# Kernel tuning notes

Hardware: AMD Instinct MI355X
Metric: run time of the kernel (lower is better)

## Reference

```python
import jax, jax.numpy as jnp
import numpy as np


def setup_inputs() -> dict:
    key = jax.random.key(0)
    k1, k2 = jax.random.split(key)
    A, B, N, M, K = 8, 16, 1024, 1024, 64
    u = jax.random.normal(k1, (A, B, N, K), dtype=jnp.float32)
    v = jax.random.normal(k2, (A, B, M, K), dtype=jnp.float32)
    return {"u": u, "v": v}


def reference(u, v):
    # to_norm = u @ v^T has shape (A,B,N,M); we only need its row/col sums.
    # sum over M of (u @ v^T) = u @ sum_m(v);  sum over N = v @ sum_n(u).
    v_sum = v.sum(axis=2)                     # (A,B,K)
    u_sum = u.sum(axis=2)                     # (A,B,K)
    row_sum = jnp.einsum('abnk,abk->abn', u, v_sum)   # to_norm.sum(dim=3)
    col_sum = jnp.einsum('abmk,abk->abm', v, u_sum)   # to_norm.sum(dim=2)
    left_mul = jax.nn.relu(jnp.sign(row_sum))[..., None]   # (A,B,N,1)
    right_mul = jax.nn.relu(jnp.sign(col_sum))[..., None]  # (A,B,M,1)
    return (left_mul * u, right_mul * v)
```

## Files before the change

### kernel.cpp

```cpp
#include <hip/hip_runtime.h>


#define NBATCH 128
#define NROW   1024
#define KDIM   64
#define ELEMS_PER_TENSOR (128ull * 1024ull * 64ull)

typedef float floatx4 __attribute__((ext_vector_type(4)));

__global__ __launch_bounds__(1024)
void fused_local_kernel(const float* __restrict__ u,
                        const float* __restrict__ v,
                        float* __restrict__ out) {
    const int bid   = blockIdx.x;
    const int batch = bid >> 1;
    const int half  = bid & 1;
    const int tid   = threadIdx.x;
    const int k4    = tid & 15;
    const int rg    = tid >> 4;
    const int wave  = tid >> 6;

    const float4* ub = (const float4*)(u + (size_t)batch * NROW * KDIM);
    const float4* vb = (const float4*)(v + (size_t)batch * NROW * KDIM);

    const int r_own0 = half * 512 + rg;
    const int r_oth0 = (1 - half) * 512 + rg;

    float4 ur[8], vr[8];
    float4 su = make_float4(0.f, 0.f, 0.f, 0.f);
    float4 sv = make_float4(0.f, 0.f, 0.f, 0.f);
    #pragma unroll
    for (int i = 0; i < 8; ++i) {
        size_t io = (size_t)(r_own0 + 64 * i) * 16 + k4;
        ur[i] = ub[io];
        vr[i] = vb[io];
        su.x += ur[i].x; su.y += ur[i].y; su.z += ur[i].z; su.w += ur[i].w;
        sv.x += vr[i].x; sv.y += vr[i].y; sv.z += vr[i].z; sv.w += vr[i].w;
    }
    #pragma unroll
    for (int i = 0; i < 8; ++i) {
        size_t ix = (size_t)(r_oth0 + 64 * i) * 16 + k4;
        float4 a = ub[ix];
        float4 b = vb[ix];
        su.x += a.x; su.y += a.y; su.z += a.z; su.w += a.w;
        sv.x += b.x; sv.y += b.y; sv.z += b.z; sv.w += b.w;
    }

    su.x += __shfl_xor(su.x, 16); su.y += __shfl_xor(su.y, 16);
    su.z += __shfl_xor(su.z, 16); su.w += __shfl_xor(su.w, 16);
    su.x += __shfl_xor(su.x, 32); su.y += __shfl_xor(su.y, 32);
    su.z += __shfl_xor(su.z, 32); su.w += __shfl_xor(su.w, 32);
    sv.x += __shfl_xor(sv.x, 16); sv.y += __shfl_xor(sv.y, 16);
    sv.z += __shfl_xor(sv.z, 16); sv.w += __shfl_xor(sv.w, 16);
    sv.x += __shfl_xor(sv.x, 32); sv.y += __shfl_xor(sv.y, 32);
    sv.z += __shfl_xor(sv.z, 32); sv.w += __shfl_xor(sv.w, 32);

    __shared__ float4 red_u[16][16];
    __shared__ float4 red_v[16][16];
    __shared__ float4 fsum[2][16];
    if ((tid & 63) < 16) {
        red_u[wave][k4] = su;
        red_v[wave][k4] = sv;
    }
    __syncthreads();

    if (tid < 32) {
        const int which = tid >> 4;
        const int c     = tid & 15;
        float4 t = make_float4(0.f, 0.f, 0.f, 0.f);
        if (which == 0) {
            #pragma unroll
            for (int i = 0; i < 16; ++i) {
                float4 b = red_v[i][c];
                t.x += b.x; t.y += b.y; t.z += b.z; t.w += b.w;
            }
        } else {
            #pragma unroll
            for (int i = 0; i < 16; ++i) {
                float4 a = red_u[i][c];
                t.x += a.x; t.y += a.y; t.z += a.z; t.w += a.w;
            }
        }
        fsum[which][c] = t;
    }
    __syncthreads();

    const float4 vs = fsum[0][k4];
    const float4 us = fsum[1][k4];

    float* ou = out + (size_t)batch * NROW * KDIM;
    float* ov = out + ELEMS_PER_TENSOR + (size_t)batch * NROW * KDIM;

    #pragma unroll
    for (int i = 0; i < 8; ++i) {
        size_t io = (size_t)(r_own0 + 64 * i) * 16 + k4;

        float pu = ur[i].x * vs.x + ur[i].y * vs.y + ur[i].z * vs.z + ur[i].w * vs.w;
        pu += __shfl_xor(pu, 1);
        pu += __shfl_xor(pu, 2);
        pu += __shfl_xor(pu, 4);
        pu += __shfl_xor(pu, 8);
        float mu = (pu > 0.f) ? 1.f : 0.f;
        floatx4 outu = { ur[i].x * mu, ur[i].y * mu, ur[i].z * mu, ur[i].w * mu };
        __builtin_nontemporal_store(outu, (floatx4*)(ou + io * 4));

        float pv = vr[i].x * us.x + vr[i].y * us.y + vr[i].z * us.z + vr[i].w * us.w;
        pv += __shfl_xor(pv, 1);
        pv += __shfl_xor(pv, 2);
        pv += __shfl_xor(pv, 4);
        pv += __shfl_xor(pv, 8);
        float mv = (pv > 0.f) ? 1.f : 0.f;
        floatx4 outv = { vr[i].x * mv, vr[i].y * mv, vr[i].z * mv, vr[i].w * mv };
        __builtin_nontemporal_store(outv, (floatx4*)(ov + io * 4));
    }
}

extern "C" void kernel_launch(void* const* d_in, const int* in_sizes, int n_in,
                              void* d_out, int out_size, void* d_ws, size_t ws_size,
                              hipStream_t stream) {
    const float* u = (const float*)d_in[0];
    const float* v = (const float*)d_in[1];
    float* out = (float*)d_out;

    fused_local_kernel<<<dim3(256), dim3(1024), 0, stream>>>(u, v, out);
}
```

Before: 118.4 us.

## Split fused kernel into column-sum and mask kernels with XCD-aware block mapping

Replaces the single fused kernel, where each block redundantly summed the other half of its batch, with a column-sum kernel that writes partial sums to workspace and a mask kernel that combines them and applies the sign mask. Block IDs are remapped so that the blocks of one batch land on the same XCD, to improve cache locality when the inputs are reread. This removes the duplicated half reads but adds a second launch and a full reread of u and v. The old fused kernel is kept as a fallback when no workspace is available.

```diff
diff --git a/kernel.cpp b/kernel.cpp
--- a/kernel.cpp
+++ b/kernel.cpp
@@ -6,42 +6,40 @@
 #define KDIM   64
 #define ELEMS_PER_TENSOR (128ull * 1024ull * 64ull)
 
+#define WS_PAYLOAD_FLOATS (NBATCH * 2 * 2 * 64)
+#define WS_BYTES ((size_t)WS_PAYLOAD_FLOATS * 4)
+
 typedef float floatx4 __attribute__((ext_vector_type(4)));
 
+__device__ __forceinline__ void decode_bid(int bid, int& batch, int& half) {
+    const int xcd  = bid & 7;
+    const int slot = bid >> 3;
+    batch = xcd * 16 + (slot >> 1);
+    half  = slot & 1;
+}
+
 __global__ __launch_bounds__(1024)
-void fused_local_kernel(const float* __restrict__ u,
-                        const float* __restrict__ v,
-                        float* __restrict__ out) {
-    const int bid   = blockIdx.x;
-    const int batch = bid >> 1;
-    const int half  = bid & 1;
-    const int tid   = threadIdx.x;
-    const int k4    = tid & 15;
-    const int rg    = tid >> 4;
-    const int wave  = tid >> 6;
+void colsum_kernel(const float* __restrict__ u,
+                   const float* __restrict__ v,
+                   float4* __restrict__ ws) {
+    int batch, half;
+    decode_bid(blockIdx.x, batch, half);
+    const int tid  = threadIdx.x;
+    const int k4   = tid & 15;
+    const int rg   = tid >> 4;
+    const int wave = tid >> 6;
 
     const float4* ub = (const float4*)(u + (size_t)batch * NROW * KDIM);
     const float4* vb = (const float4*)(v + (size_t)batch * NROW * KDIM);
-
-    const int r_own0 = half * 512 + rg;
-    const int r_oth0 = (1 - half) * 512 + rg;
-
-    float4 ur[8], vr[8];
+    const int r0 = half * 512 + rg;
+
     float4 su = make_float4(0.f, 0.f, 0.f, 0.f);
     float4 sv = make_float4(0.f, 0.f, 0.f, 0.f);
     #pragma unroll
     for (int i = 0; i < 8; ++i) {
-        size_t io = (size_t)(r_own0 + 64 * i) * 16 + k4;
-        ur[i] = ub[io];
-        vr[i] = vb[io];
-        su.x += ur[i].x; su.y += ur[i].y; su.z += ur[i].z; su.w += ur[i].w;
-        sv.x += vr[i].x; sv.y += vr[i].y; sv.z += vr[i].z; sv.w += vr[i].w;
-    }
-    #pragma unroll
-    for (int i = 0; i < 8; ++i) {
-        size_t ix = (size_t)(r_oth0 + 64 * i) * 16 + k4;
-        float4 a = ub[ix];
-        float4 b = vb[ix];
+        size_t io = (size_t)(r0 + 64 * i) * 16 + k4;
+        float4 a = ub[io];
+        float4 b = vb[io];
         su.x += a.x; su.y += a.y; su.z += a.z; su.w += a.w;
         sv.x += b.x; sv.y += b.y; sv.z += b.z; sv.w += b.w;
     }
@@ -57,7 +55,6 @@
 
     __shared__ float4 red_u[16][16];
     __shared__ float4 red_v[16][16];
-    __shared__ float4 fsum[2][16];
     if ((tid & 63) < 16) {
         red_u[wave][k4] = su;
         red_v[wave][k4] = sv;
@@ -81,20 +78,44 @@
                 t.x += a.x; t.y += a.y; t.z += a.z; t.w += a.w;
             }
         }
-        fsum[which][c] = t;
-    }
-    __syncthreads();
-
-    const float4 vs = fsum[0][k4];
-    const float4 us = fsum[1][k4];
-
-    float* ou = out + (size_t)batch * NROW * KDIM;
-    float* ov = out + ELEMS_PER_TENSOR + (size_t)batch * NROW * KDIM;
-
-    #pragma unroll
-    for (int i = 0; i < 8; ++i) {
-        size_t io = (size_t)(r_own0 + 64 * i) * 16 + k4;
-
+        ws[(((size_t)batch * 2 + half) * 2 + which) * 16 + c] = t;
+    }
+}
+
+__global__ __launch_bounds__(1024)
+void mask_kernel(const float* __restrict__ u,
+                 const float* __restrict__ v,
+                 float* __restrict__ out,
+                 const float4* __restrict__ ws) {
+    int batch, half;
+    decode_bid(blockIdx.x, batch, half);
+    const int tid = threadIdx.x;
+    const int k4  = tid & 15;
+    const int rg  = tid >> 4;
+
+    const float4 vs0 = ws[(((size_t)batch * 2 + 0) * 2 + 0) * 16 + k4];
+    const float4 vs1 = ws[(((size_t)batch * 2 + 1) * 2 + 0) * 16 + k4];
+    const float4 us0 = ws[(((size_t)batch * 2 + 0) * 2 + 1) * 16 + k4];
+    const float4 us1 = ws[(((size_t)batch * 2 + 1) * 2 + 1) * 16 + k4];
+    const float4 vs = make_float4(vs0.x + vs1.x, vs0.y + vs1.y,
+                                  vs0.z + vs1.z, vs0.w + vs1.w);
+    const float4 us = make_float4(us0.x + us1.x, us0.y + us1.y,
+                                  us0.z + us1.z, us0.w + us1.w);
+
+    const size_t boff = (size_t)batch * NROW * KDIM;
+    const float4* ub = (const float4*)(u + boff);
+    const float4* vb = (const float4*)(v + boff);
+    float* ou = out + boff;
+    float* ov = out + ELEMS_PER_TENSOR + boff;
+    const int r0 = half * 512 + rg;
+
+    float4 ur[8];
+    #pragma unroll
+    for (int i = 0; i < 8; ++i)
+        ur[i] = ub[(size_t)(r0 + 64 * i) * 16 + k4];
+    #pragma unroll
+    for (int i = 0; i < 8; ++i) {
+        size_t io = (size_t)(r0 + 64 * i) * 16 + k4;
         float pu = ur[i].x * vs.x + ur[i].y * vs.y + ur[i].z * vs.z + ur[i].w * vs.w;
         pu += __shfl_xor(pu, 1);
         pu += __shfl_xor(pu, 2);
@@ -103,7 +124,15 @@
         float mu = (pu > 0.f) ? 1.f : 0.f;
         floatx4 outu = { ur[i].x * mu, ur[i].y * mu, ur[i].z * mu, ur[i].w * mu };
         __builtin_nontemporal_store(outu, (floatx4*)(ou + io * 4));
-
+    }
+
+    float4 vr[8];
+    #pragma unroll
+    for (int i = 0; i < 8; ++i)
+        vr[i] = vb[(size_t)(r0 + 64 * i) * 16 + k4];
+    #pragma unroll
+    for (int i = 0; i < 8; ++i) {
+        size_t io = (size_t)(r0 + 64 * i) * 16 + k4;
         float pv = vr[i].x * us.x + vr[i].y * us.y + vr[i].z * us.z + vr[i].w * us.w;
         pv += __shfl_xor(pv, 1);
         pv += __shfl_xor(pv, 2);
@@ -115,6 +144,112 @@
     }
 }
 
+__global__ __launch_bounds__(1024)
+void fused_local_kernel(const float* __restrict__ u,
+                        const float* __restrict__ v,
+                        float* __restrict__ out) {
+    int batch, half;
+    decode_bid(blockIdx.x, batch, half);
+    const int tid  = threadIdx.x;
+    const int k4   = tid & 15;
+    const int rg   = tid >> 4;
+    const int wave = tid >> 6;
+
+    const float4* ub = (const float4*)(u + (size_t)batch * NROW * KDIM);
+    const float4* vb = (const float4*)(v + (size_t)batch * NROW * KDIM);
+
+    const int r_own0 = half * 512 + rg;
+    const int r_oth0 = (1 - half) * 512 + rg;
+
+    float4 ur[8], vr[8];
+    float4 su = make_float4(0.f, 0.f, 0.f, 0.f);
+    float4 sv = make_float4(0.f, 0.f, 0.f, 0.f);
+    #pragma unroll
+    for (int i = 0; i < 8; ++i) {
+        size_t io = (size_t)(r_own0 + 64 * i) * 16 + k4;
+        ur[i] = ub[io];
+        vr[i] = vb[io];
+        su.x += ur[i].x; su.y += ur[i].y; su.z += ur[i].z; su.w += ur[i].w;
+        sv.x += vr[i].x; sv.y += vr[i].y; sv.z += vr[i].z; sv.w += vr[i].w;
+    }
+    #pragma unroll
+    for (int i = 0; i < 8; ++i) {
+        size_t ix = (size_t)(r_oth0 + 64 * i) * 16 + k4;
+        float4 a = ub[ix];
+        float4 b = vb[ix];
+        su.x += a.x; su.y += a.y; su.z += a.z; su.w += a.w;
+        sv.x += b.x; sv.y += b.y; sv.z += b.z; sv.w += b.w;
+    }
+
+    su.x += __shfl_xor(su.x, 16); su.y += __shfl_xor(su.y, 16);
+    su.z += __shfl_xor(su.z, 16); su.w += __shfl_xor(su.w, 16);
+    su.x += __shfl_xor(su.x, 32); su.y += __shfl_xor(su.y, 32);
+    su.z += __shfl_xor(su.z, 32); su.w += __shfl_xor(su.w, 32);
+    sv.x += __shfl_xor(sv.x, 16); sv.y += __shfl_xor(sv.y, 16);
+    sv.z += __shfl_xor(sv.z, 16); sv.w += __shfl_xor(sv.w, 16);
+    sv.x += __shfl_xor(sv.x, 32); sv.y += __shfl_xor(sv.y, 32);
+    sv.z += __shfl_xor(sv.z, 32); sv.w += __shfl_xor(sv.w, 32);
+
+    __shared__ float4 red_u[16][16];
+    __shared__ float4 red_v[16][16];
+    __shared__ float4 fsum[2][16];
+    if ((tid & 63) < 16) {
+        red_u[wave][k4] = su;
+        red_v[wave][k4] = sv;
+    }
+    __syncthreads();
+
+    if (tid < 32) {
+        const int which = tid >> 4;
+        const int c     = tid & 15;
+        float4 t = make_float4(0.f, 0.f, 0.f, 0.f);
+        if (which == 0) {
+            #pragma unroll
+            for (int i = 0; i < 16; ++i) {
+                float4 b = red_v[i][c];
+                t.x += b.x; t.y += b.y; t.z += b.z; t.w += b.w;
+            }
+        } else {
+            #pragma unroll
+            for (int i = 0; i < 16; ++i) {
+                float4 a = red_u[i][c];
+                t.x += a.x; t.y += a.y; t.z += a.z; t.w += a.w;
+            }
+        }
+        fsum[which][c] = t;
+    }
+    __syncthreads();
+
+    const float4 vs = fsum[0][k4];
+    const float4 us = fsum[1][k4];
+
+    float* ou = out + (size_t)batch * NROW * KDIM;
+    float* ov = out + ELEMS_PER_TENSOR + (size_t)batch * NROW * KDIM;
+
+    #pragma unroll
+    for (int i = 0; i < 8; ++i) {
+        size_t io = (size_t)(r_own0 + 64 * i) * 16 + k4;
+
+        float pu = ur[i].x * vs.x + ur[i].y * vs.y + ur[i].z * vs.z + ur[i].w * vs.w;
+        pu += __shfl_xor(pu, 1);
+        pu += __shfl_xor(pu, 2);
+        pu += __shfl_xor(pu, 4);
+        pu += __shfl_xor(pu, 8);
+        float mu = (pu > 0.f) ? 1.f : 0.f;
+        floatx4 outu = { ur[i].x * mu, ur[i].y * mu, ur[i].z * mu, ur[i].w * mu };
+        __builtin_nontemporal_store(outu, (floatx4*)(ou + io * 4));
+
+        float pv = vr[i].x * us.x + vr[i].y * us.y + vr[i].z * us.z + vr[i].w * us.w;
+        pv += __shfl_xor(pv, 1);
+        pv += __shfl_xor(pv, 2);
+        pv += __shfl_xor(pv, 4);
+        pv += __shfl_xor(pv, 8);
+        float mv = (pv > 0.f) ? 1.f : 0.f;
+        floatx4 outv = { vr[i].x * mv, vr[i].y * mv, vr[i].z * mv, vr[i].w * mv };
+        __builtin_nontemporal_store(outv, (floatx4*)(ov + io * 4));
+    }
+}
+
 extern "C" void kernel_launch(void* const* d_in, const int* in_sizes, int n_in,
                               void* d_out, int out_size, void* d_ws, size_t ws_size,
                               hipStream_t stream) {
@@ -122,5 +257,11 @@
     const float* v = (const float*)d_in[1];
     float* out = (float*)d_out;
 
-    fused_local_kernel<<<dim3(256), dim3(1024), 0, stream>>>(u, v, out);
-}
+    if (d_ws != nullptr && ws_size >= WS_BYTES) {
+        float4* ws = (float4*)d_ws;
+        colsum_kernel<<<dim3(256), dim3(1024), 0, stream>>>(u, v, ws);
+        mask_kernel<<<dim3(256), dim3(1024), 0, stream>>>(u, v, out, ws);
+    } else {
+        fused_local_kernel<<<dim3(256), dim3(1024), 0, stream>>>(u, v, out);
+    }
+}
```

Result: no change. 118.2 us (-0.1%).
